# Performance work log

Measured on AMD Instinct MI355X. Metric: run time of the kernel, lower is better.

Reference implementation:

```python
import jax, jax.numpy as jnp
import numpy as np

N = 50000
D = 64
K_POS = 32
K_NEG = 64


def setup_inputs() -> dict:
    key = jax.random.key(0)
    ks = jax.random.split(key, 7)
    return {
        "P": jax.random.normal(ks[0], (N, D), dtype=jnp.float32),
        "W_d": jax.random.normal(ks[1], (D,), dtype=jnp.float32),
        "deg_vec": jax.random.uniform(ks[2], (N,), dtype=jnp.float32),
        "pos_idx": jax.random.randint(ks[3], (N, K_POS), 0, N, dtype=jnp.int32),
        "neg_idx": jax.random.randint(ks[4], (N, K_NEG), 0, N, dtype=jnp.int32),
        "deg_pos_idx": jax.random.randint(ks[5], (N, K_POS), 0, N, dtype=jnp.int32),
        "deg_neg_idx": jax.random.randint(ks[6], (N, K_NEG), 0, N, dtype=jnp.int32),
    }


def _contrast(Z, pos, neg):
    # hamming_dist(zi, zp) = sum_d |zi - zp|  (per node i over its index list)
    Hp = jnp.abs(Z[:, None, :] - Z[pos]).sum(-1)  # [N, K_pos]
    Hn = jnp.abs(Z[:, None, :] - Z[neg]).sum(-1)  # [N, K_neg]
    # softmax_formula: -( mean_p H_pos - log sum_n exp(H_neg) ), summed over nodes
    per_node = Hp.mean(-1) - jax.nn.logsumexp(Hn, axis=-1)
    return -per_node.sum()


def reference(P, W_d, deg_vec, pos_idx, neg_idx, deg_pos_idx, deg_neg_idx):
    Z = jax.nn.sigmoid(P)  # Sigmoid_alt assumed elementwise logistic sigmoid
    L_adj = _contrast(Z, pos_idx, neg_idx)
    L_deg_dist = _contrast(Z, deg_pos_idx, deg_neg_idx)
    # degree_loss: MSE(Z @ W_d, deg_vec)
    L_deg = jnp.mean((Z @ W_d - deg_vec) ** 2)
    return (L_adj, L_deg_dist, L_deg)
```

## Files before the change

### kernel.cpp

```cpp
#include <hip/hip_runtime.h>
#include <stdint.h>

#define NDIM 64
#define KPOS 32
#define KNEG 64

__global__ __launch_bounds__(256) void pe_sig_deg_kernel(
    const float* __restrict__ P,
    const float* __restrict__ Wd,
    const float* __restrict__ deg,
    uint8_t* __restrict__ Zq,
    float* __restrict__ out,
    int N) {
  const int lane = threadIdx.x & 63;
  const int wid  = threadIdx.x >> 6;
  const int nwaves = (gridDim.x * blockDim.x) >> 6;
  int gw = (blockIdx.x * blockDim.x + threadIdx.x) >> 6;

  const float wd = Wd[lane];
  float acc = 0.f;
  for (int i = gw; i < N; i += nwaves) {
    float p = P[(size_t)i * NDIM + lane];
    float z = 1.f / (1.f + __expf(-p));
    Zq[(size_t)i * NDIM + lane] = (uint8_t)(z * 255.f + 0.5f);
    float dot = z * wd;
    #pragma unroll
    for (int off = 32; off; off >>= 1) dot += __shfl_xor(dot, off);
    float d = dot - deg[i];
    acc += d * d;
  }
  __shared__ float sacc[4];
  if (lane == 0) sacc[wid] = acc;
  __syncthreads();
  if (threadIdx.x == 0) {
    atomicAdd(out + 2, (sacc[0] + sacc[1] + sacc[2] + sacc[3]) * (1.0f / (float)N));
  }
}

__device__ __forceinline__ unsigned sad16(uint4 a, uint4 b, unsigned acc) {
  acc = __builtin_amdgcn_sad_u8(a.x, b.x, acc);
  acc = __builtin_amdgcn_sad_u8(a.y, b.y, acc);
  acc = __builtin_amdgcn_sad_u8(a.z, b.z, acc);
  acc = __builtin_amdgcn_sad_u8(a.w, b.w, acc);
  return acc;
}

__device__ __forceinline__ float contrast_u8(
    const uint8_t* __restrict__ Zq, uint4 zi,
    int p0, int p1, int n0, int n1, int n2, int n3,
    int c, unsigned* posacc) {
  const size_t off = (size_t)c * 16;
  const uint4 rp0 = *(const uint4*)(Zq + (size_t)p0 * NDIM + off);
  const uint4 rp1 = *(const uint4*)(Zq + (size_t)p1 * NDIM + off);
  const uint4 rn0 = *(const uint4*)(Zq + (size_t)n0 * NDIM + off);
  const uint4 rn1 = *(const uint4*)(Zq + (size_t)n1 * NDIM + off);
  const uint4 rn2 = *(const uint4*)(Zq + (size_t)n2 * NDIM + off);
  const uint4 rn3 = *(const uint4*)(Zq + (size_t)n3 * NDIM + off);

  *posacc = sad16(rp0, zi, sad16(rp1, zi, *posacc));

  int h0 = (int)sad16(rn0, zi, 0u);
  int h1 = (int)sad16(rn1, zi, 0u);
  int h2 = (int)sad16(rn2, zi, 0u);
  int h3 = (int)sad16(rn3, zi, 0u);
  h0 += __shfl_xor(h0, 1); h0 += __shfl_xor(h0, 2);
  h1 += __shfl_xor(h1, 1); h1 += __shfl_xor(h1, 2);
  h2 += __shfl_xor(h2, 1); h2 += __shfl_xor(h2, 2);
  h3 += __shfl_xor(h3, 1); h3 += __shfl_xor(h3, 2);

  int m = max(max(h0, h1), max(h2, h3));
  #pragma unroll
  for (int o = 4; o < 64; o <<= 1) m = max(m, __shfl_xor(m, o));

  const float s = 1.4426950408889634f / 255.f;
  float e = exp2f((float)(h0 - m) * s) + exp2f((float)(h1 - m) * s) +
            exp2f((float)(h2 - m) * s) + exp2f((float)(h3 - m) * s);
  #pragma unroll
  for (int o = 4; o < 64; o <<= 1) e += __shfl_xor(e, o);

  return (float)m * (1.f / 255.f) + __logf(e);
}

struct Idx { int p0, p1, n0, n1, n2, n3, q0, q1, m0, m1, m2, m3; };

__device__ __forceinline__ Idx load_idx(
    const int* __restrict__ pos, const int* __restrict__ neg,
    const int* __restrict__ dpos, const int* __restrict__ dneg, int i, int q) {
  Idx d;
  const int* pr = pos  + (size_t)i * KPOS;
  const int* nr = neg  + (size_t)i * KNEG;
  const int* qr = dpos + (size_t)i * KPOS;
  const int* mr = dneg + (size_t)i * KNEG;
  d.p0 = pr[q]; d.p1 = pr[16 + q];
  d.n0 = nr[q]; d.n1 = nr[16 + q]; d.n2 = nr[32 + q]; d.n3 = nr[48 + q];
  d.q0 = qr[q]; d.q1 = qr[16 + q];
  d.m0 = mr[q]; d.m1 = mr[16 + q]; d.m2 = mr[32 + q]; d.m3 = mr[48 + q];
  return d;
}

__global__ __launch_bounds__(256) void pe_contrast_kernel(
    const uint8_t* __restrict__ Zq,
    const int* __restrict__ pos_idx,
    const int* __restrict__ neg_idx,
    const int* __restrict__ dpos_idx,
    const int* __restrict__ dneg_idx,
    float* __restrict__ out,
    int N) {
  const int lane = threadIdx.x & 63;
  const int q = lane >> 2, c = lane & 3;
  const int wid  = threadIdx.x >> 6;
  const int nwaves = (gridDim.x * blockDim.x) >> 6;
  const int gw = (blockIdx.x * blockDim.x + threadIdx.x) >> 6;

  float l1 = 0.f, l2 = 0.f;
  unsigned pa1 = 0u, pa2 = 0u;

  int i = gw;
  Idx cur;
  if (i < N) cur = load_idx(pos_idx, neg_idx, dpos_idx, dneg_idx, i, q);
  while (i < N) {
    const int inext = i + nwaves;
    Idx nxt = cur;
    if (inext < N) nxt = load_idx(pos_idx, neg_idx, dpos_idx, dneg_idx, inext, q);

    const uint4 zi = *(const uint4*)(Zq + (size_t)i * NDIM + (size_t)c * 16);
    l1 += contrast_u8(Zq, zi, cur.p0, cur.p1, cur.n0, cur.n1, cur.n2, cur.n3, c, &pa1);
    l2 += contrast_u8(Zq, zi, cur.q0, cur.q1, cur.m0, cur.m1, cur.m2, cur.m3, c, &pa2);

    i = inext;
    cur = nxt;
  }

  int p1s = (int)pa1, p2s = (int)pa2;
  #pragma unroll
  for (int o = 1; o < 64; o <<= 1) { p1s += __shfl_xor(p1s, o); p2s += __shfl_xor(p2s, o); }

  const float pscale = 1.f / (255.f * (float)KPOS);
  const float c1 = l1 - (float)p1s * pscale;
  const float c2 = l2 - (float)p2s * pscale;

  __shared__ float s1[4], s2[4];
  if (lane == 0) { s1[wid] = c1; s2[wid] = c2; }
  __syncthreads();
  if (threadIdx.x == 0) {
    atomicAdd(out + 0, s1[0] + s1[1] + s1[2] + s1[3]);
    atomicAdd(out + 1, s2[0] + s2[1] + s2[2] + s2[3]);
  }
}

extern "C" void kernel_launch(void* const* d_in, const int* in_sizes, int n_in,
                              void* d_out, int out_size, void* d_ws, size_t ws_size,
                              hipStream_t stream) {
  const float* P       = (const float*)d_in[0];
  const float* Wd      = (const float*)d_in[1];
  const float* deg     = (const float*)d_in[2];
  const int*   pos_idx = (const int*)d_in[3];
  const int*   neg_idx = (const int*)d_in[4];
  const int*   dpos    = (const int*)d_in[5];
  const int*   dneg    = (const int*)d_in[6];
  float* out = (float*)d_out;

  const int N = in_sizes[2];
  uint8_t* Zq = (uint8_t*)d_ws;

  hipMemsetAsync(out, 0, (size_t)out_size * sizeof(float), stream);

  pe_sig_deg_kernel<<<1024, 256, 0, stream>>>(P, Wd, deg, Zq, out, N);
  pe_contrast_kernel<<<2048, 256, 0, stream>>>(Zq, pos_idx, neg_idx, dpos, dneg, out, N);
}
```

Baseline: 101.7 us.

## Drop logsumexp max pass, batch all gathers upfront, use 32-bit addressing

The contrast kernel now issues all twelve row gathers for both losses before doing any arithmetic, and interleaves the shuffle reductions of the two losses. This exposes more memory-level parallelism and ILP. It also removes the max-subtraction step of logsumexp, relying on Hamming distances being bounded so exp cannot overflow, which saves one cross-lane max reduction per node. Addresses switch from 64-bit to 32-bit unsigned arithmetic, and the sigmoid kernel grid is doubled. The cost is higher register pressure and weaker numerical safety if distances ever grow large.

After: 111.4 us. 1.1x slower.

```diff
diff --git a/kernel.cpp b/kernel.cpp
--- a/kernel.cpp
+++ b/kernel.cpp
@@ -20,9 +20,9 @@
   const float wd = Wd[lane];
   float acc = 0.f;
   for (int i = gw; i < N; i += nwaves) {
-    float p = P[(size_t)i * NDIM + lane];
+    float p = P[(unsigned)i * NDIM + lane];
     float z = 1.f / (1.f + __expf(-p));
-    Zq[(size_t)i * NDIM + lane] = (uint8_t)(z * 255.f + 0.5f);
+    Zq[((unsigned)i << 6) | lane] = (uint8_t)(z * 255.f + 0.5f);
     float dot = z * wd;
     #pragma unroll
     for (int off = 32; off; off >>= 1) dot += __shfl_xor(dot, off);
@@ -45,52 +45,17 @@
   return acc;
 }
 
-__device__ __forceinline__ float contrast_u8(
-    const uint8_t* __restrict__ Zq, uint4 zi,
-    int p0, int p1, int n0, int n1, int n2, int n3,
-    int c, unsigned* posacc) {
-  const size_t off = (size_t)c * 16;
-  const uint4 rp0 = *(const uint4*)(Zq + (size_t)p0 * NDIM + off);
-  const uint4 rp1 = *(const uint4*)(Zq + (size_t)p1 * NDIM + off);
-  const uint4 rn0 = *(const uint4*)(Zq + (size_t)n0 * NDIM + off);
-  const uint4 rn1 = *(const uint4*)(Zq + (size_t)n1 * NDIM + off);
-  const uint4 rn2 = *(const uint4*)(Zq + (size_t)n2 * NDIM + off);
-  const uint4 rn3 = *(const uint4*)(Zq + (size_t)n3 * NDIM + off);
-
-  *posacc = sad16(rp0, zi, sad16(rp1, zi, *posacc));
-
-  int h0 = (int)sad16(rn0, zi, 0u);
-  int h1 = (int)sad16(rn1, zi, 0u);
-  int h2 = (int)sad16(rn2, zi, 0u);
-  int h3 = (int)sad16(rn3, zi, 0u);
-  h0 += __shfl_xor(h0, 1); h0 += __shfl_xor(h0, 2);
-  h1 += __shfl_xor(h1, 1); h1 += __shfl_xor(h1, 2);
-  h2 += __shfl_xor(h2, 1); h2 += __shfl_xor(h2, 2);
-  h3 += __shfl_xor(h3, 1); h3 += __shfl_xor(h3, 2);
-
-  int m = max(max(h0, h1), max(h2, h3));
-  #pragma unroll
-  for (int o = 4; o < 64; o <<= 1) m = max(m, __shfl_xor(m, o));
-
-  const float s = 1.4426950408889634f / 255.f;
-  float e = exp2f((float)(h0 - m) * s) + exp2f((float)(h1 - m) * s) +
-            exp2f((float)(h2 - m) * s) + exp2f((float)(h3 - m) * s);
-  #pragma unroll
-  for (int o = 4; o < 64; o <<= 1) e += __shfl_xor(e, o);
-
-  return (float)m * (1.f / 255.f) + __logf(e);
-}
-
 struct Idx { int p0, p1, n0, n1, n2, n3, q0, q1, m0, m1, m2, m3; };
 
 __device__ __forceinline__ Idx load_idx(
     const int* __restrict__ pos, const int* __restrict__ neg,
-    const int* __restrict__ dpos, const int* __restrict__ dneg, int i, int q) {
+    const int* __restrict__ dpos, const int* __restrict__ dneg,
+    unsigned i, int q) {
   Idx d;
-  const int* pr = pos  + (size_t)i * KPOS;
-  const int* nr = neg  + (size_t)i * KNEG;
-  const int* qr = dpos + (size_t)i * KPOS;
-  const int* mr = dneg + (size_t)i * KNEG;
+  const int* pr = pos  + i * KPOS;
+  const int* nr = neg  + i * KNEG;
+  const int* qr = dpos + i * KPOS;
+  const int* mr = dneg + i * KNEG;
   d.p0 = pr[q]; d.p1 = pr[16 + q];
   d.n0 = nr[q]; d.n1 = nr[16 + q]; d.n2 = nr[32 + q]; d.n3 = nr[48 + q];
   d.q0 = qr[q]; d.q1 = qr[16 + q];
@@ -112,20 +77,57 @@
   const int nwaves = (gridDim.x * blockDim.x) >> 6;
   const int gw = (blockIdx.x * blockDim.x + threadIdx.x) >> 6;
 
+  const unsigned coff = (unsigned)c << 4;
+  #define ZROW(j) (*(const uint4*)(Zq + ((((unsigned)(j)) << 6) | coff)))
+
   float l1 = 0.f, l2 = 0.f;
   unsigned pa1 = 0u, pa2 = 0u;
+  const float S = 1.4426950408889634f / 255.f;
 
   int i = gw;
   Idx cur;
-  if (i < N) cur = load_idx(pos_idx, neg_idx, dpos_idx, dneg_idx, i, q);
+  if (i < N) cur = load_idx(pos_idx, neg_idx, dpos_idx, dneg_idx, (unsigned)i, q);
   while (i < N) {
+    const uint4 zi  = ZROW(i);
+    const uint4 rp0 = ZROW(cur.p0), rp1 = ZROW(cur.p1);
+    const uint4 rn0 = ZROW(cur.n0), rn1 = ZROW(cur.n1);
+    const uint4 rn2 = ZROW(cur.n2), rn3 = ZROW(cur.n3);
+    const uint4 rq0 = ZROW(cur.q0), rq1 = ZROW(cur.q1);
+    const uint4 rm0 = ZROW(cur.m0), rm1 = ZROW(cur.m1);
+    const uint4 rm2 = ZROW(cur.m2), rm3 = ZROW(cur.m3);
+
     const int inext = i + nwaves;
     Idx nxt = cur;
-    if (inext < N) nxt = load_idx(pos_idx, neg_idx, dpos_idx, dneg_idx, inext, q);
+    if (inext < N) nxt = load_idx(pos_idx, neg_idx, dpos_idx, dneg_idx, (unsigned)inext, q);
 
-    const uint4 zi = *(const uint4*)(Zq + (size_t)i * NDIM + (size_t)c * 16);
-    l1 += contrast_u8(Zq, zi, cur.p0, cur.p1, cur.n0, cur.n1, cur.n2, cur.n3, c, &pa1);
-    l2 += contrast_u8(Zq, zi, cur.q0, cur.q1, cur.m0, cur.m1, cur.m2, cur.m3, c, &pa2);
+    pa1 = sad16(rp0, zi, sad16(rp1, zi, pa1));
+    pa2 = sad16(rq0, zi, sad16(rq1, zi, pa2));
+
+    int h0 = (int)sad16(rn0, zi, 0u), h1 = (int)sad16(rn1, zi, 0u);
+    int h2 = (int)sad16(rn2, zi, 0u), h3 = (int)sad16(rn3, zi, 0u);
+    int g0 = (int)sad16(rm0, zi, 0u), g1 = (int)sad16(rm1, zi, 0u);
+    int g2 = (int)sad16(rm2, zi, 0u), g3 = (int)sad16(rm3, zi, 0u);
+
+    h0 += __shfl_xor(h0, 1); h1 += __shfl_xor(h1, 1);
+    h2 += __shfl_xor(h2, 1); h3 += __shfl_xor(h3, 1);
+    g0 += __shfl_xor(g0, 1); g1 += __shfl_xor(g1, 1);
+    g2 += __shfl_xor(g2, 1); g3 += __shfl_xor(g3, 1);
+    h0 += __shfl_xor(h0, 2); h1 += __shfl_xor(h1, 2);
+    h2 += __shfl_xor(h2, 2); h3 += __shfl_xor(h3, 2);
+    g0 += __shfl_xor(g0, 2); g1 += __shfl_xor(g1, 2);
+    g2 += __shfl_xor(g2, 2); g3 += __shfl_xor(g3, 2);
+
+    float e1 = exp2f((float)h0 * S) + exp2f((float)h1 * S) +
+               exp2f((float)h2 * S) + exp2f((float)h3 * S);
+    float e2 = exp2f((float)g0 * S) + exp2f((float)g1 * S) +
+               exp2f((float)g2 * S) + exp2f((float)g3 * S);
+    #pragma unroll
+    for (int o = 4; o < 64; o <<= 1) {
+      e1 += __shfl_xor(e1, o);
+      e2 += __shfl_xor(e2, o);
+    }
+    l1 += __logf(e1);
+    l2 += __logf(e2);
 
     i = inext;
     cur = nxt;
@@ -146,6 +148,7 @@
     atomicAdd(out + 0, s1[0] + s1[1] + s1[2] + s1[3]);
     atomicAdd(out + 1, s2[0] + s2[1] + s2[2] + s2[3]);
   }
+  #undef ZROW
 }
 
 extern "C" void kernel_launch(void* const* d_in, const int* in_sizes, int n_in,
@@ -165,6 +168,6 @@
 
   hipMemsetAsync(out, 0, (size_t)out_size * sizeof(float), stream);
 
-  pe_sig_deg_kernel<<<1024, 256, 0, stream>>>(P, Wd, deg, Zq, out, N);
+  pe_sig_deg_kernel<<<2048, 256, 0, stream>>>(P, Wd, deg, Zq, out, N);
   pe_contrast_kernel<<<2048, 256, 0, stream>>>(Zq, pos_idx, neg_idx, dpos, dneg, out, N);
 }
```
